# Performance work log

Hardware: AMD Instinct MI355X
Metric: run time of the kernel (lower is better)

Reference implementation:

```python
import jax, jax.numpy as jnp
import numpy as np


def setup_inputs() -> dict:
    key = jax.random.key(0)
    k1, k2 = jax.random.split(key)
    src = jax.random.normal(k1, (4096, 1024, 3), dtype=jnp.float32)
    tgt = jax.random.normal(k2, (4096, 1024, 3), dtype=jnp.float32)
    return {"src": src, "tgt": tgt}


def reference(src, tgt):
    # src, tgt: [bs, N, 3] -> work in [bs, 3, N] like the torch module
    src_t = jnp.swapaxes(src, 1, 2)                      # [bs, 3, N]
    tgt_t = jnp.swapaxes(tgt, 1, 2)                      # [bs, 3, N]
    src_mean = src_t.mean(axis=2, keepdims=True)         # [bs, 3, 1]
    tgt_mean = tgt_t.mean(axis=2, keepdims=True)         # [bs, 3, 1]
    src_c = src_t - src_mean                             # [bs, 3, N]
    tgt_c = tgt_t - tgt_mean                             # [bs, 3, N]
    # Cross-covariance H = src_c @ tgt_c^T : [bs, 3, 3]
    H = jnp.einsum('bin,bjn->bij', src_c, tgt_c)
    u, s, vh = jnp.linalg.svd(H)                         # H = u diag(s) vh
    v = jnp.swapaxes(vh, 1, 2)                           # torch.svd's v
    ut = jnp.swapaxes(u, 1, 2)
    R0 = jnp.matmul(v, ut)                               # candidate rotation
    det = jnp.linalg.det(R0)                             # [bs]
    # If det < 0, multiply v by reflect=diag(1,1,-1), i.e. negate last column of v
    sign = jnp.where(det < 0, -1.0, 1.0).astype(src.dtype)  # [bs]
    col_scale = jnp.stack(
        [jnp.ones_like(sign), jnp.ones_like(sign), sign], axis=-1
    )[:, None, :]                                        # [bs, 1, 3]
    R = jnp.matmul(v * col_scale, ut)                    # [bs, 3, 3]
    t = (-jnp.matmul(R, src_mean) + tgt_mean)[..., 0]    # [bs, 3]
    return (R, t)
```

## Files before the change

### kernel.cpp

```cpp
#include <hip/hip_runtime.h>
#include <math.h>

constexpr int NPTS = 1024;
constexpr int WPB = 4;

__global__ __launch_bounds__(256) void reduce_kernel(
    const float* __restrict__ src, const float* __restrict__ tgt,
    float* __restrict__ ws, int nbatch)
{
    const int wave = threadIdx.x >> 6;
    const int lane = threadIdx.x & 63;
    const int b = blockIdx.x * WPB + wave;
    if (b >= nbatch) return;

    const size_t base = (size_t)b * (NPTS * 3);

    float acc[15];
#pragma unroll
    for (int i = 0; i < 15; ++i) acc[i] = 0.f;

#pragma unroll
    for (int j = 0; j < 4; ++j) {
        const int g = j * 64 + lane;
        const float* sp = src + base + g * 12;
        const float* tp = tgt + base + g * 12;
        float4 sA = *(const float4*)(sp + 0);
        float4 sB = *(const float4*)(sp + 4);
        float4 sC = *(const float4*)(sp + 8);
        float4 tA = *(const float4*)(tp + 0);
        float4 tB = *(const float4*)(tp + 4);
        float4 tC = *(const float4*)(tp + 8);

        float sx[4] = {sA.x, sA.w, sB.z, sC.y};
        float sy[4] = {sA.y, sB.x, sB.w, sC.z};
        float sz[4] = {sA.z, sB.y, sC.x, sC.w};
        float tx[4] = {tA.x, tA.w, tB.z, tC.y};
        float ty[4] = {tA.y, tB.x, tB.w, tC.z};
        float tz[4] = {tA.z, tB.y, tC.x, tC.w};

#pragma unroll
        for (int k = 0; k < 4; ++k) {
            acc[0] += sx[k]; acc[1] += sy[k]; acc[2] += sz[k];
            acc[3] += tx[k]; acc[4] += ty[k]; acc[5] += tz[k];
            acc[6]  += sx[k] * tx[k]; acc[7]  += sx[k] * ty[k]; acc[8]  += sx[k] * tz[k];
            acc[9]  += sy[k] * tx[k]; acc[10] += sy[k] * ty[k]; acc[11] += sy[k] * tz[k];
            acc[12] += sz[k] * tx[k]; acc[13] += sz[k] * ty[k]; acc[14] += sz[k] * tz[k];
        }
    }

#pragma unroll
    for (int off = 32; off >= 1; off >>= 1) {
#pragma unroll
        for (int i = 0; i < 15; ++i)
            acc[i] += __shfl_down(acc[i], off, 64);
    }

    if (lane == 0) {
        float4* w = (float4*)(ws + (size_t)b * 16);
        w[0] = make_float4(acc[0],  acc[1],  acc[2],  acc[3]);
        w[1] = make_float4(acc[4],  acc[5],  acc[6],  acc[7]);
        w[2] = make_float4(acc[8],  acc[9],  acc[10], acc[11]);
        w[3] = make_float4(acc[12], acc[13], acc[14], 0.f);
    }
}

__device__ __forceinline__ float frcp(float x)  { return __builtin_amdgcn_rcpf(x); }
__device__ __forceinline__ float frsq(float x)  { return __builtin_amdgcn_rsqf(x); }
__device__ __forceinline__ float fsqrt(float x) { return __builtin_amdgcn_sqrtf(x); }

__global__ __launch_bounds__(256) void svd_kernel(
    const float* __restrict__ ws, float* __restrict__ out, int nbatch)
{
    const int b = blockIdx.x * 256 + threadIdx.x;
    if (b >= nbatch) return;

    const float4* w = (const float4*)(ws + (size_t)b * 16);
    float4 w0 = w[0], w1 = w[1], w2 = w[2], w3 = w[3];
    float r[15] = {w0.x, w0.y, w0.z, w0.w,
                   w1.x, w1.y, w1.z, w1.w,
                   w2.x, w2.y, w2.z, w2.w,
                   w3.x, w3.y, w3.z};

    const float invN = 1.0f / (float)NPTS;
    float mus[3] = {r[0] * invN, r[1] * invN, r[2] * invN};
    float mut[3] = {r[3] * invN, r[4] * invN, r[5] * invN};

    float H[3][3];
#pragma unroll
    for (int i = 0; i < 3; ++i)
#pragma unroll
        for (int j = 0; j < 3; ++j)
            H[i][j] = r[6 + i * 3 + j] - (float)NPTS * mus[i] * mut[j];

    float A[3][3];
#pragma unroll
    for (int i = 0; i < 3; ++i)
#pragma unroll
        for (int j = 0; j < 3; ++j)
            A[i][j] = H[0][i] * H[0][j] + H[1][i] * H[1][j] + H[2][i] * H[2][j];

    float V[3][3] = {{1.f, 0.f, 0.f}, {0.f, 1.f, 0.f}, {0.f, 0.f, 1.f}};
    auto rot = [&](int p, int q) {
        float apq = A[p][q];
        float diff = A[q][q] - A[p][p];
        float theta = diff * frcp(2.0f * apq);
        float t = copysignf(frcp(fabsf(theta) + fsqrt(fmaf(theta, theta, 1.0f))), theta);
        t = (fabsf(apq) < 1e-20f) ? 0.0f : t;
        float c = frsq(fmaf(t, t, 1.0f));
        float s = t * c;
#pragma unroll
        for (int k = 0; k < 3; ++k) {
            float akp = A[k][p], akq = A[k][q];
            A[k][p] = c * akp - s * akq;
            A[k][q] = s * akp + c * akq;
        }
#pragma unroll
        for (int k = 0; k < 3; ++k) {
            float apk = A[p][k], aqk = A[q][k];
            A[p][k] = c * apk - s * aqk;
            A[q][k] = s * apk + c * aqk;
        }
#pragma unroll
        for (int k = 0; k < 3; ++k) {
            float vkp = V[k][p], vkq = V[k][q];
            V[k][p] = c * vkp - s * vkq;
            V[k][q] = s * vkp + c * vkq;
        }
    };
#pragma unroll
    for (int sweep = 0; sweep < 5; ++sweep) {
        rot(0, 1);
        rot(0, 2);
        rot(1, 2);
    }

    float l0 = A[0][0], l1 = A[1][1], l2 = A[2][2];
    float e0[3] = {V[0][0], V[1][0], V[2][0]};
    float e1[3] = {V[0][1], V[1][1], V[2][1]};
    float e2[3] = {V[0][2], V[1][2], V[2][2]};
    auto cswap = [](float& la, float* va, float& lb, float* vb) {
        bool sw = lb > la;
        float tl = sw ? lb : la;
        lb = sw ? la : lb;
        la = tl;
#pragma unroll
        for (int k = 0; k < 3; ++k) {
            float tv = sw ? vb[k] : va[k];
            vb[k] = sw ? va[k] : vb[k];
            va[k] = tv;
        }
    };
    cswap(l0, e0, l1, e1);
    cswap(l0, e0, l2, e2);
    cswap(l1, e1, l2, e2);

    float *v1 = e0, *v2 = e1, *v3 = e2;

    float u1[3], u2[3], u3[3], hv[3];
    hv[0] = H[0][0]*v1[0] + H[0][1]*v1[1] + H[0][2]*v1[2];
    hv[1] = H[1][0]*v1[0] + H[1][1]*v1[1] + H[1][2]*v1[2];
    hv[2] = H[2][0]*v1[0] + H[2][1]*v1[1] + H[2][2]*v1[2];
    {
        float n = frsq(fmaf(hv[0], hv[0], fmaf(hv[1], hv[1], hv[2]*hv[2])) + 1e-30f);
        u1[0] = hv[0] * n; u1[1] = hv[1] * n; u1[2] = hv[2] * n;
    }
    hv[0] = H[0][0]*v2[0] + H[0][1]*v2[1] + H[0][2]*v2[2];
    hv[1] = H[1][0]*v2[0] + H[1][1]*v2[1] + H[1][2]*v2[2];
    hv[2] = H[2][0]*v2[0] + H[2][1]*v2[1] + H[2][2]*v2[2];
    {
        float d = u1[0]*hv[0] + u1[1]*hv[1] + u1[2]*hv[2];
        hv[0] -= d * u1[0]; hv[1] -= d * u1[1]; hv[2] -= d * u1[2];
        float n = frsq(fmaf(hv[0], hv[0], fmaf(hv[1], hv[1], hv[2]*hv[2])) + 1e-30f);
        u2[0] = hv[0] * n; u2[1] = hv[1] * n; u2[2] = hv[2] * n;
    }
    u3[0] = u1[1]*u2[2] - u1[2]*u2[1];
    u3[1] = u1[2]*u2[0] - u1[0]*u2[2];
    u3[2] = u1[0]*u2[1] - u1[1]*u2[0];

    float cx = v1[1]*v2[2] - v1[2]*v2[1];
    float cy = v1[2]*v2[0] - v1[0]*v2[2];
    float cz = v1[0]*v2[1] - v1[1]*v2[0];
    float detV = cx * v3[0] + cy * v3[1] + cz * v3[2];
    float d3 = (detV < 0.f) ? -1.f : 1.f;

    float R[3][3];
#pragma unroll
    for (int i = 0; i < 3; ++i)
#pragma unroll
        for (int j = 0; j < 3; ++j)
            R[i][j] = v1[i]*u1[j] + v2[i]*u2[j] + d3 * v3[i]*u3[j];

    float tvec[3];
#pragma unroll
    for (int i = 0; i < 3; ++i)
        tvec[i] = mut[i] - (R[i][0]*mus[0] + R[i][1]*mus[1] + R[i][2]*mus[2]);

    float* Rout = out + (size_t)b * 9;
#pragma unroll
    for (int i = 0; i < 3; ++i)
#pragma unroll
        for (int j = 0; j < 3; ++j)
            Rout[i * 3 + j] = R[i][j];
    float* tout = out + (size_t)nbatch * 9 + (size_t)b * 3;
#pragma unroll
    for (int i = 0; i < 3; ++i) tout[i] = tvec[i];
}

extern "C" void kernel_launch(void* const* d_in, const int* in_sizes, int n_in,
                              void* d_out, int out_size, void* d_ws, size_t ws_size,
                              hipStream_t stream) {
    const float* src = (const float*)d_in[0];
    const float* tgt = (const float*)d_in[1];
    float* out = (float*)d_out;
    float* ws = (float*)d_ws;
    const int nbatch = in_sizes[0] / (NPTS * 3);

    const int nblocksA = (nbatch + WPB - 1) / WPB;
    reduce_kernel<<<nblocksA, 256, 0, stream>>>(src, tgt, ws, nbatch);

    const int nblocksB = (nbatch + 255) / 256;
    svd_kernel<<<nblocksB, 256, 0, stream>>>(ws, out, nbatch);
}
```

Before: 24.91 us.

## Fuse reduction and SVD kernels using last-block atomic counter handoff

```diff
diff --git a/kernel.cpp b/kernel.cpp
--- a/kernel.cpp
+++ b/kernel.cpp
@@ -3,77 +3,15 @@
 
 constexpr int NPTS = 1024;
 constexpr int WPB = 4;
-
-__global__ __launch_bounds__(256) void reduce_kernel(
-    const float* __restrict__ src, const float* __restrict__ tgt,
-    float* __restrict__ ws, int nbatch)
-{
-    const int wave = threadIdx.x >> 6;
-    const int lane = threadIdx.x & 63;
-    const int b = blockIdx.x * WPB + wave;
-    if (b >= nbatch) return;
-
-    const size_t base = (size_t)b * (NPTS * 3);
-
-    float acc[15];
-#pragma unroll
-    for (int i = 0; i < 15; ++i) acc[i] = 0.f;
-
-#pragma unroll
-    for (int j = 0; j < 4; ++j) {
-        const int g = j * 64 + lane;
-        const float* sp = src + base + g * 12;
-        const float* tp = tgt + base + g * 12;
-        float4 sA = *(const float4*)(sp + 0);
-        float4 sB = *(const float4*)(sp + 4);
-        float4 sC = *(const float4*)(sp + 8);
-        float4 tA = *(const float4*)(tp + 0);
-        float4 tB = *(const float4*)(tp + 4);
-        float4 tC = *(const float4*)(tp + 8);
-
-        float sx[4] = {sA.x, sA.w, sB.z, sC.y};
-        float sy[4] = {sA.y, sB.x, sB.w, sC.z};
-        float sz[4] = {sA.z, sB.y, sC.x, sC.w};
-        float tx[4] = {tA.x, tA.w, tB.z, tC.y};
-        float ty[4] = {tA.y, tB.x, tB.w, tC.z};
-        float tz[4] = {tA.z, tB.y, tC.x, tC.w};
-
-#pragma unroll
-        for (int k = 0; k < 4; ++k) {
-            acc[0] += sx[k]; acc[1] += sy[k]; acc[2] += sz[k];
-            acc[3] += tx[k]; acc[4] += ty[k]; acc[5] += tz[k];
-            acc[6]  += sx[k] * tx[k]; acc[7]  += sx[k] * ty[k]; acc[8]  += sx[k] * tz[k];
-            acc[9]  += sy[k] * tx[k]; acc[10] += sy[k] * ty[k]; acc[11] += sy[k] * tz[k];
-            acc[12] += sz[k] * tx[k]; acc[13] += sz[k] * ty[k]; acc[14] += sz[k] * tz[k];
-        }
-    }
-
-#pragma unroll
-    for (int off = 32; off >= 1; off >>= 1) {
-#pragma unroll
-        for (int i = 0; i < 15; ++i)
-            acc[i] += __shfl_down(acc[i], off, 64);
-    }
-
-    if (lane == 0) {
-        float4* w = (float4*)(ws + (size_t)b * 16);
-        w[0] = make_float4(acc[0],  acc[1],  acc[2],  acc[3]);
-        w[1] = make_float4(acc[4],  acc[5],  acc[6],  acc[7]);
-        w[2] = make_float4(acc[8],  acc[9],  acc[10], acc[11]);
-        w[3] = make_float4(acc[12], acc[13], acc[14], 0.f);
-    }
-}
 
 __device__ __forceinline__ float frcp(float x)  { return __builtin_amdgcn_rcpf(x); }
 __device__ __forceinline__ float frsq(float x)  { return __builtin_amdgcn_rsqf(x); }
 __device__ __forceinline__ float fsqrt(float x) { return __builtin_amdgcn_sqrtf(x); }
 
-__global__ __launch_bounds__(256) void svd_kernel(
-    const float* __restrict__ ws, float* __restrict__ out, int nbatch)
+__device__ __forceinline__ void svd_solve(const float* __restrict__ ws,
+                                          float* __restrict__ out,
+                                          int b, int nbatch)
 {
-    const int b = blockIdx.x * 256 + threadIdx.x;
-    if (b >= nbatch) return;
-
     const float4* w = (const float4*)(ws + (size_t)b * 16);
     float4 w0 = w[0], w1 = w[1], w2 = w[2], w3 = w[3];
     float r[15] = {w0.x, w0.y, w0.z, w0.w,
@@ -206,6 +144,89 @@
     for (int i = 0; i < 3; ++i) tout[i] = tvec[i];
 }
 
+__global__ __launch_bounds__(256) void kabsch_fused(
+    const float* __restrict__ src, const float* __restrict__ tgt,
+    float* __restrict__ ws, unsigned* __restrict__ cnt,
+    float* __restrict__ out, int nbatch, int nblocks, int cons_threshold)
+{
+    const int wave = threadIdx.x >> 6;
+    const int lane = threadIdx.x & 63;
+    const int b = blockIdx.x * WPB + wave;
+
+    float acc[15];
+#pragma unroll
+    for (int i = 0; i < 15; ++i) acc[i] = 0.f;
+
+    if (b < nbatch) {
+        const size_t base = (size_t)b * (NPTS * 3);
+#pragma unroll
+        for (int j = 0; j < 4; ++j) {
+            const int g = j * 64 + lane;
+            const float* sp = src + base + g * 12;
+            const float* tp = tgt + base + g * 12;
+            float4 sA = *(const float4*)(sp + 0);
+            float4 sB = *(const float4*)(sp + 4);
+            float4 sC = *(const float4*)(sp + 8);
+            float4 tA = *(const float4*)(tp + 0);
+            float4 tB = *(const float4*)(tp + 4);
+            float4 tC = *(const float4*)(tp + 8);
+
+            float sx[4] = {sA.x, sA.w, sB.z, sC.y};
+            float sy[4] = {sA.y, sB.x, sB.w, sC.z};
+            float sz[4] = {sA.z, sB.y, sC.x, sC.w};
+            float tx[4] = {tA.x, tA.w, tB.z, tC.y};
+            float ty[4] = {tA.y, tB.x, tB.w, tC.z};
+            float tz[4] = {tA.z, tB.y, tC.x, tC.w};
+
+#pragma unroll
+            for (int k = 0; k < 4; ++k) {
+                acc[0] += sx[k]; acc[1] += sy[k]; acc[2] += sz[k];
+                acc[3] += tx[k]; acc[4] += ty[k]; acc[5] += tz[k];
+                acc[6]  += sx[k] * tx[k]; acc[7]  += sx[k] * ty[k]; acc[8]  += sx[k] * tz[k];
+                acc[9]  += sy[k] * tx[k]; acc[10] += sy[k] * ty[k]; acc[11] += sy[k] * tz[k];
+                acc[12] += sz[k] * tx[k]; acc[13] += sz[k] * ty[k]; acc[14] += sz[k] * tz[k];
+            }
+        }
+    }
+
+#pragma unroll
+    for (int off = 32; off >= 1; off >>= 1) {
+#pragma unroll
+        for (int i = 0; i < 15; ++i)
+            acc[i] += __shfl_down(acc[i], off, 64);
+    }
+
+    if (b < nbatch && lane == 0) {
+        float4* w = (float4*)(ws + (size_t)b * 16);
+        w[0] = make_float4(acc[0],  acc[1],  acc[2],  acc[3]);
+        w[1] = make_float4(acc[4],  acc[5],  acc[6],  acc[7]);
+        w[2] = make_float4(acc[8],  acc[9],  acc[10], acc[11]);
+        w[3] = make_float4(acc[12], acc[13], acc[14], 0.f);
+    }
+
+    __shared__ unsigned s_old;
+    __syncthreads();
+    if (threadIdx.x == 0) {
+        s_old = __hip_atomic_fetch_add(cnt, 1u, __ATOMIC_RELEASE,
+                                       __HIP_MEMORY_SCOPE_AGENT);
+    }
+    __syncthreads();
+    const unsigned old = s_old;
+    if ((int)old < cons_threshold) return;
+
+    if (threadIdx.x == 0) {
+        while (__hip_atomic_load(cnt, __ATOMIC_ACQUIRE,
+                                 __HIP_MEMORY_SCOPE_AGENT) < (unsigned)nblocks)
+            __builtin_amdgcn_s_sleep(2);
+    }
+    __syncthreads();
+
+    const int chunk = (int)old - cons_threshold;
+    const int sb = chunk * 256 + threadIdx.x;
+    if (sb < nbatch)
+        svd_solve(ws, out, sb, nbatch);
+}
+
 extern "C" void kernel_launch(void* const* d_in, const int* in_sizes, int n_in,
                               void* d_out, int out_size, void* d_ws, size_t ws_size,
                               hipStream_t stream) {
@@ -215,9 +236,12 @@
     float* ws = (float*)d_ws;
     const int nbatch = in_sizes[0] / (NPTS * 3);
 
-    const int nblocksA = (nbatch + WPB - 1) / WPB;
-    reduce_kernel<<<nblocksA, 256, 0, stream>>>(src, tgt, ws, nbatch);
-
-    const int nblocksB = (nbatch + 255) / 256;
-    svd_kernel<<<nblocksB, 256, 0, stream>>>(ws, out, nbatch);
+    unsigned* cnt = (unsigned*)(ws + (size_t)nbatch * 16);
+    hipMemsetAsync(cnt, 0, sizeof(unsigned), stream);
+
+    const int nblocks = (nbatch + WPB - 1) / WPB;
+    const int ncons = (nbatch + 255) / 256;
+    const int cons_threshold = nblocks - ncons;
+    kabsch_fused<<<nblocks, 256, 0, stream>>>(src, tgt, ws, cnt, out,
+                                              nbatch, nblocks, cons_threshold);
 }
```

Result: slower. 56.83 us (+128.1%).
